# Kernel tuning notes

Hardware: AMD Instinct MI355X
Metric: run time of the kernel (lower is better)

## Reference

```python
import jax, jax.numpy as jnp
import numpy as np

D_MODEL = 1024
NUM_HEADS = 16
WINDOW = 128
DEPTH = D_MODEL // NUM_HEADS


def setup_inputs() -> dict:
    key = jax.random.key(0)
    ks = jax.random.split(key, 9)
    B, S = 2, 2048
    scale = 1.0 / np.sqrt(D_MODEL)
    x = jax.random.normal(ks[0], (B, S, D_MODEL), dtype=jnp.float32)
    Wq = jax.random.normal(ks[1], (D_MODEL, D_MODEL), dtype=jnp.float32) * scale
    Wk = jax.random.normal(ks[2], (D_MODEL, D_MODEL), dtype=jnp.float32) * scale
    Wv = jax.random.normal(ks[3], (D_MODEL, D_MODEL), dtype=jnp.float32) * scale
    Wo = jax.random.normal(ks[4], (D_MODEL, D_MODEL), dtype=jnp.float32) * scale
    bq = jnp.zeros((D_MODEL,), jnp.float32)
    bk = jnp.zeros((D_MODEL,), jnp.float32)
    bv = jnp.zeros((D_MODEL,), jnp.float32)
    bo = jnp.zeros((D_MODEL,), jnp.float32)
    return {"x": x, "Wq": Wq, "bq": bq, "Wk": Wk, "bk": bk,
            "Wv": Wv, "bv": bv, "Wo": Wo, "bo": bo}


def _split_heads(t, B, S):
    # [B,S,D] -> [B,H,S,depth]
    return t.reshape(B, S, NUM_HEADS, DEPTH).transpose(0, 2, 1, 3)


def reference(x, Wq, bq, Wk, bk, Wv, bv, Wo, bo):
    B, S, _ = x.shape
    q = _split_heads(x @ Wq + bq, B, S)
    k = _split_heads(x @ Wk + bk, B, S)
    v = _split_heads(x @ Wv + bv, B, S)
    scores = jnp.einsum('bhqd,bhkd->bhqk', q, k) / jnp.sqrt(jnp.float32(DEPTH))
    idx = jnp.arange(S)
    # mask[i_row=j, i_col=i] per original: |i - j| <= window (symmetric)
    local = jnp.abs(idx[None, :] - idx[:, None]) <= WINDOW  # [S,S]
    scores = jnp.where(local[None, None], scores, jnp.float32(-1e9))
    attn = jax.nn.softmax(scores, axis=-1)
    out = jnp.einsum('bhqk,bhkd->bhqd', attn, v)
    concat = out.transpose(0, 2, 1, 3).reshape(B, S, D_MODEL)
    return concat @ Wo + bo
```

## Files before the change

### kernel.cpp

```cpp
#include <hip/hip_runtime.h>
#include <cstdint>
#include <cstddef>

typedef __attribute__((ext_vector_type(8))) short short8;
typedef __attribute__((ext_vector_type(4))) short short4v;
typedef __attribute__((ext_vector_type(4))) float f32x4;
typedef short8 bf16x8;

typedef __attribute__((address_space(1))) const unsigned GU;
typedef __attribute__((address_space(3))) unsigned LU;

__device__ __forceinline__ short f2bf(float f) {
  unsigned u = __builtin_bit_cast(unsigned, f);
  u += 0x7fffu + ((u >> 16) & 1u);
  return (short)(u >> 16);
}

__global__ __launch_bounds__(256) void k_cast_x(const float* __restrict__ x, short* __restrict__ xb) {
  size_t i = ((size_t)blockIdx.x * 256 + threadIdx.x) * 8;
  f32x4 a = *(const f32x4*)(x + i);
  f32x4 b = *(const f32x4*)(x + i + 4);
  short8 o;
#pragma unroll
  for (int j = 0; j < 4; ++j) { o[j] = f2bf(a[j]); o[4 + j] = f2bf(b[j]); }
  *(short8*)(xb + i) = o;
}

__global__ __launch_bounds__(256) void k_tw(const float* __restrict__ W0, const float* __restrict__ W1,
                                            const float* __restrict__ W2, const float* __restrict__ W3,
                                            short* __restrict__ WT) {
  __shared__ short T[64 * 72];
  int bid = blockIdx.x;
  int widx = bid >> 8;
  int t = bid & 255;
  int kr = (t >> 4) * 64, nc = (t & 15) * 64;
  const float* W = widx == 0 ? W0 : widx == 1 ? W1 : widx == 2 ? W2 : W3;
  short* out = WT + (size_t)widx * 1048576;
  int tid = threadIdx.x;
#pragma unroll
  for (int i = 0; i < 4; ++i) {
    int idx = tid + i * 256;
    int k = idx >> 4, n4 = (idx & 15) << 2;
    f32x4 v = *(const f32x4*)(W + (size_t)(kr + k) * 1024 + nc + n4);
#pragma unroll
    for (int j = 0; j < 4; ++j) T[(n4 + j) * 72 + k] = f2bf(v[j]);
  }
  __syncthreads();
#pragma unroll
  for (int i = 0; i < 2; ++i) {
    int idx = tid + i * 256;
    int n = idx >> 3, k8 = (idx & 7) << 3;
    *(short8*)(out + (size_t)(nc + n) * 1024 + kr + k8) = *(const short8*)&T[n * 72 + k8];
  }
}

__global__ __launch_bounds__(256) void k_tv(const short* __restrict__ v, short* __restrict__ vT) {
  __shared__ short T[64 * 72];
  int bid = blockIdx.x;
  int stile = bid & 31, h = (bid >> 5) & 15, b = bid >> 9;
  int s0 = stile * 64;
  int tid = threadIdx.x;
#pragma unroll
  for (int i = 0; i < 2; ++i) {
    int idx = tid + i * 256;
    int s = idx >> 3, d0 = (idx & 7) << 3;
    short8 vec = *(const short8*)(v + ((size_t)b * 2048 + s0 + s) * 1024 + h * 64 + d0);
#pragma unroll
    for (int j = 0; j < 8; ++j) T[(d0 + j) * 72 + s] = vec[j];
  }
  __syncthreads();
#pragma unroll
  for (int i = 0; i < 2; ++i) {
    int idx = tid + i * 256;
    int d = idx >> 3, s8 = (idx & 7) << 3;
    *(short8*)(vT + (((size_t)b * 16 + h) * 64 + d) * 2048 + s0 + s8) = *(const short8*)&T[d * 72 + s8];
  }
}

template <int MODE>
__global__ __launch_bounds__(256, 2) void k_gemm(
    const short* __restrict__ A, const short* __restrict__ BT,
    const float* __restrict__ bias0, const float* __restrict__ bias1, const float* __restrict__ bias2,
    short* __restrict__ outb, float* __restrict__ outf) {
  __shared__ short As[2][128 * 32];
  __shared__ short Bs[2][128 * 32];
  const int tid = threadIdx.x;
  const int lane = tid & 63, w = tid >> 6;
  const int g = lane >> 4, qi = lane & 15;
  const int wr = (w >> 1) * 64, wc = (w & 1) * 64;
  const int m0 = blockIdx.y * 128, n0 = blockIdx.x * 128;
  const size_t K = 1024;
  const short* Ab = A + (size_t)m0 * K;
  const short* Bb = BT + (size_t)n0 * K;

  auto stage = [&](int buf, int k0) {
#pragma unroll
    for (int i = 0; i < 2; ++i) {
      int cidx = tid + i * 256;
      int r = cidx >> 2, c = (cidx & 3) << 3;
      __builtin_amdgcn_global_load_lds((GU*)(Ab + (size_t)r * K + k0 + c),
                                       (LU*)(&As[buf][cidx * 8]), 16, 0, 0);
      __builtin_amdgcn_global_load_lds((GU*)(Bb + (size_t)r * K + k0 + c),
                                       (LU*)(&Bs[buf][cidx * 8]), 16, 0, 0);
    }
  };

  f32x4 acc[4][4];
#pragma unroll
  for (int i = 0; i < 4; ++i)
#pragma unroll
    for (int j = 0; j < 4; ++j) acc[i][j] = (f32x4)(0.0f);

  stage(0, 0);
  __syncthreads();
  for (int kt = 0; kt < 32; ++kt) {
    int cur = kt & 1;
    if (kt < 31) stage(cur ^ 1, (kt + 1) * 32);
    bf16x8 a[4], b[4];
#pragma unroll
    for (int mf = 0; mf < 4; ++mf)
      a[mf] = *(const bf16x8*)&As[cur][(wr + mf * 16 + qi) * 32 + g * 8];
#pragma unroll
    for (int nf = 0; nf < 4; ++nf)
      b[nf] = *(const bf16x8*)&Bs[cur][(wc + nf * 16 + qi) * 32 + g * 8];
#pragma unroll
    for (int mf = 0; mf < 4; ++mf)
#pragma unroll
      for (int nf = 0; nf < 4; ++nf)
        acc[mf][nf] = __builtin_amdgcn_mfma_f32_16x16x32_bf16(a[mf], b[nf], acc[mf][nf], 0, 0, 0);
    __syncthreads();
  }

  if (MODE == 0) {
    int sel = n0 >> 10;
    const float* bias = sel == 0 ? bias0 : (sel == 1 ? bias1 : bias2);
    size_t outoff = (size_t)sel * 4194304;
#pragma unroll
    for (int nf = 0; nf < 4; ++nf) {
      int col = n0 + wc + nf * 16 + qi;
      int cl = col & 1023;
      float bv = bias[cl];
#pragma unroll
      for (int mf = 0; mf < 4; ++mf) {
        int row = m0 + wr + mf * 16 + g * 4;
#pragma unroll
        for (int j = 0; j < 4; ++j)
          outb[outoff + (size_t)(row + j) * 1024 + cl] = f2bf(acc[mf][nf][j] + bv);
      }
    }
  } else {
#pragma unroll
    for (int nf = 0; nf < 4; ++nf) {
      int col = n0 + wc + nf * 16 + qi;
      float bv = bias0[col];
#pragma unroll
      for (int mf = 0; mf < 4; ++mf) {
        int row = m0 + wr + mf * 16 + g * 4;
#pragma unroll
        for (int j = 0; j < 4; ++j)
          outf[(size_t)(row + j) * 1024 + col] = acc[mf][nf][j] + bv;
      }
    }
  }
}

__global__ __launch_bounds__(256, 2) void k_attn(const short* __restrict__ qg_,
                                                 const short* __restrict__ kg_,
                                                 const short* __restrict__ vT,
                                                 short* __restrict__ outp) {
  __shared__ short Qs[64 * 72];
  __shared__ short Ks[64 * 72];
  __shared__ short Vs[64 * 72];
  __shared__ short Ps[4][16 * 72];
  int bid = blockIdx.x;
  int qt = bid & 31, h = (bid >> 5) & 15, b = bid >> 9;
  int q0 = qt * 64;
  int tid = threadIdx.x, lane = tid & 63, w = tid >> 6;
  int g = lane >> 4, qi = lane & 15;

  const short* qsrc = qg_ + ((size_t)b * 2048 + q0) * 1024 + h * 64;
#pragma unroll
  for (int i = 0; i < 2; ++i) {
    int idx = tid + i * 256;
    int r = idx >> 3, c = (idx & 7) << 3;
    *(short8*)&Qs[r * 72 + c] = *(const short8*)&qsrc[(size_t)r * 1024 + c];
  }

  float m = -1e30f, l = 0.f;
  f32x4 oacc[4];
#pragma unroll
  for (int i = 0; i < 4; ++i) oacc[i] = (f32x4)(0.0f);
  int qglob = q0 + w * 16 + qi;

  for (int cc = 0; cc < 5; ++cc) {
    int kb0 = q0 - 128 + cc * 64;
    if (kb0 < 0 || kb0 >= 2048) continue;
    __syncthreads();
    const short* ksrc = kg_ + ((size_t)b * 2048 + kb0) * 1024 + h * 64;
    const short* vsrc = vT + ((size_t)(b * 16 + h)) * 64 * 2048 + kb0;
#pragma unroll
    for (int i = 0; i < 2; ++i) {
      int idx = tid + i * 256;
      int r = idx >> 3, c = (idx & 7) << 3;
      *(short8*)&Ks[r * 72 + c] = *(const short8*)&ksrc[(size_t)r * 1024 + c];
      *(short8*)&Vs[r * 72 + c] = *(const short8*)&vsrc[(size_t)r * 2048 + c];
    }
    __syncthreads();

    f32x4 st[4];
#pragma unroll
    for (int i = 0; i < 4; ++i) st[i] = (f32x4)(0.0f);
#pragma unroll
    for (int ds = 0; ds < 2; ++ds) {
      bf16x8 qf = *(const bf16x8*)&Qs[(w * 16 + qi) * 72 + ds * 32 + g * 8];
#pragma unroll
      for (int mf = 0; mf < 4; ++mf) {
        bf16x8 kf = *(const bf16x8*)&Ks[(mf * 16 + qi) * 72 + ds * 32 + g * 8];
        st[mf] = __builtin_amdgcn_mfma_f32_16x16x32_bf16(kf, qf, st[mf], 0, 0, 0);
      }
    }

    float pv[16];
    float pm = -1e30f;
#pragma unroll
    for (int mf = 0; mf < 4; ++mf)
#pragma unroll
      for (int j = 0; j < 4; ++j) {
        int kcol = kb0 + mf * 16 + g * 4 + j;
        float s = st[mf][j] * 0.125f;
        int d = kcol - qglob;
        bool valid = (d >= -128) && (d <= 128);
        s = valid ? s : -1e30f;
        pv[mf * 4 + j] = s;
        pm = fmaxf(pm, s);
      }
    pm = fmaxf(pm, __shfl_xor(pm, 16));
    pm = fmaxf(pm, __shfl_xor(pm, 32));
    float mnew = fmaxf(m, pm);
    float scale = __expf(m - mnew);
    float ls = 0.f;
#pragma unroll
    for (int e = 0; e < 16; ++e) {
      float p = pv[e] > -1e29f ? __expf(pv[e] - mnew) : 0.f;
      pv[e] = p;
      ls += p;
    }
    ls += __shfl_xor(ls, 16);
    ls += __shfl_xor(ls, 32);
    l = l * scale + ls;
    m = mnew;
#pragma unroll
    for (int mf = 0; mf < 4; ++mf) oacc[mf] *= scale;

#pragma unroll
    for (int f = 0; f < 4; ++f) {
      short4v pk;
#pragma unroll
      for (int j = 0; j < 4; ++j) pk[j] = f2bf(pv[f * 4 + j]);
      *(short4v*)&Ps[w][qi * 72 + f * 16 + g * 4] = pk;
    }

#pragma unroll
    for (int ks = 0; ks < 2; ++ks) {
      bf16x8 pf = *(const bf16x8*)&Ps[w][qi * 72 + ks * 32 + g * 8];
#pragma unroll
      for (int mf = 0; mf < 4; ++mf) {
        bf16x8 vf = *(const bf16x8*)&Vs[(mf * 16 + qi) * 72 + ks * 32 + g * 8];
        oacc[mf] = __builtin_amdgcn_mfma_f32_16x16x32_bf16(vf, pf, oacc[mf], 0, 0, 0);
      }
    }
  }

  __syncthreads();
  short* Os = Ks;
  float inv = 1.f / l;
#pragma unroll
  for (int mf = 0; mf < 4; ++mf) {
    short4v pk;
#pragma unroll
    for (int j = 0; j < 4; ++j) pk[j] = f2bf(oacc[mf][j] * inv);
    *(short4v*)&Os[(w * 16 + qi) * 72 + mf * 16 + g * 4] = pk;
  }
  __syncthreads();
  short* dst = outp + ((size_t)b * 2048 + q0) * 1024 + h * 64;
  int r = tid >> 2, c16 = (tid & 3) << 4;
  *(short8*)&dst[(size_t)r * 1024 + c16] = *(const short8*)&Os[r * 72 + c16];
  *(short8*)&dst[(size_t)r * 1024 + c16 + 8] = *(const short8*)&Os[r * 72 + c16 + 8];
}

extern "C" void kernel_launch(void* const* d_in, const int* in_sizes, int n_in,
                              void* d_out, int out_size, void* d_ws, size_t ws_size,
                              hipStream_t stream) {
  const float* x  = (const float*)d_in[0];
  const float* Wq = (const float*)d_in[1];
  const float* bq = (const float*)d_in[2];
  const float* Wk = (const float*)d_in[3];
  const float* bk = (const float*)d_in[4];
  const float* Wv = (const float*)d_in[5];
  const float* bv = (const float*)d_in[6];
  const float* Wo = (const float*)d_in[7];
  const float* bo = (const float*)d_in[8];

  short* ws = (short*)d_ws;
  short* xb       = ws;
  short* qkv      = ws + 4194304;
  short* vbuf     = qkv + 2 * 4194304;
  short* vT       = ws;
  short* attn_out = vbuf;
  short* WT       = ws + 4 * 4194304;

  k_cast_x<<<2048, 256, 0, stream>>>(x, xb);
  k_tw<<<1024, 256, 0, stream>>>(Wq, Wk, Wv, Wo, WT);
  {
    dim3 grid(24, 32);
    k_gemm<0><<<grid, 256, 0, stream>>>(xb, WT, bq, bk, bv, qkv, nullptr);
  }
  k_tv<<<1024, 256, 0, stream>>>(vbuf, vT);
  k_attn<<<1024, 256, 0, stream>>>(qkv, qkv + 4194304, vT, attn_out);
  {
    dim3 grid(8, 32);
    k_gemm<1><<<grid, 256, 0, stream>>>(attn_out, WT + 3 * 1048576, bo, bo, bo, nullptr, (float*)d_out);
  }
}
```

Before: 100.4 us.

## Swizzle GEMM LDS tiles and stage epilogue through LDS for coalesced stores

```diff
diff --git a/kernel.cpp b/kernel.cpp
--- a/kernel.cpp
+++ b/kernel.cpp
@@ -82,8 +82,7 @@
     const short* __restrict__ A, const short* __restrict__ BT,
     const float* __restrict__ bias0, const float* __restrict__ bias1, const float* __restrict__ bias2,
     short* __restrict__ outb, float* __restrict__ outf) {
-  __shared__ short As[2][128 * 32];
-  __shared__ short Bs[2][128 * 32];
+  __shared__ short Smem[16384];
   const int tid = threadIdx.x;
   const int lane = tid & 63, w = tid >> 6;
   const int g = lane >> 4, qi = lane & 15;
@@ -94,14 +93,17 @@
   const short* Bb = BT + (size_t)n0 * K;
 
   auto stage = [&](int buf, int k0) {
+    short* Asb = Smem + buf * 4096;
+    short* Bsb = Smem + 8192 + buf * 4096;
 #pragma unroll
     for (int i = 0; i < 2; ++i) {
       int cidx = tid + i * 256;
-      int r = cidx >> 2, c = (cidx & 3) << 3;
-      __builtin_amdgcn_global_load_lds((GU*)(Ab + (size_t)r * K + k0 + c),
-                                       (LU*)(&As[buf][cidx * 8]), 16, 0, 0);
-      __builtin_amdgcn_global_load_lds((GU*)(Bb + (size_t)r * K + k0 + c),
-                                       (LU*)(&Bs[buf][cidx * 8]), 16, 0, 0);
+      int r = cidx >> 2;
+      int csw = ((cidx & 3) ^ ((r >> 1) & 3)) << 3;
+      __builtin_amdgcn_global_load_lds((GU*)(Ab + (size_t)r * K + k0 + csw),
+                                       (LU*)(&Asb[cidx * 8]), 16, 0, 0);
+      __builtin_amdgcn_global_load_lds((GU*)(Bb + (size_t)r * K + k0 + csw),
+                                       (LU*)(&Bsb[cidx * 8]), 16, 0, 0);
     }
   };
 
@@ -116,13 +118,19 @@
   for (int kt = 0; kt < 32; ++kt) {
     int cur = kt & 1;
     if (kt < 31) stage(cur ^ 1, (kt + 1) * 32);
+    const short* Asb = Smem + cur * 4096;
+    const short* Bsb = Smem + 8192 + cur * 4096;
     bf16x8 a[4], b[4];
 #pragma unroll
-    for (int mf = 0; mf < 4; ++mf)
-      a[mf] = *(const bf16x8*)&As[cur][(wr + mf * 16 + qi) * 32 + g * 8];
-#pragma unroll
-    for (int nf = 0; nf < 4; ++nf)
-      b[nf] = *(const bf16x8*)&Bs[cur][(wc + nf * 16 + qi) * 32 + g * 8];
+    for (int mf = 0; mf < 4; ++mf) {
+      int R = wr + mf * 16 + qi;
+      a[mf] = *(const bf16x8*)&Asb[R * 32 + ((g ^ ((R >> 1) & 3)) << 3)];
+    }
+#pragma unroll
+    for (int nf = 0; nf < 4; ++nf) {
+      int R = wc + nf * 16 + qi;
+      b[nf] = *(const bf16x8*)&Bsb[R * 32 + ((g ^ ((R >> 1) & 3)) << 3)];
+    }
 #pragma unroll
     for (int mf = 0; mf < 4; ++mf)
 #pragma unroll
@@ -135,30 +143,48 @@
     int sel = n0 >> 10;
     const float* bias = sel == 0 ? bias0 : (sel == 1 ? bias1 : bias2);
     size_t outoff = (size_t)sel * 4194304;
-#pragma unroll
-    for (int nf = 0; nf < 4; ++nf) {
-      int col = n0 + wc + nf * 16 + qi;
-      int cl = col & 1023;
-      float bv = bias[cl];
-#pragma unroll
-      for (int mf = 0; mf < 4; ++mf) {
-        int row = m0 + wr + mf * 16 + g * 4;
+    int ncol0 = n0 & 1023;
+    float bv[4];
+#pragma unroll
+    for (int nf = 0; nf < 4; ++nf) bv[nf] = bias[ncol0 + wc + nf * 16 + qi];
+    short* Os = Smem;
+#pragma unroll
+    for (int mf = 0; mf < 4; ++mf) {
+      __syncthreads();
+#pragma unroll
+      for (int nf = 0; nf < 4; ++nf)
 #pragma unroll
         for (int j = 0; j < 4; ++j)
-          outb[outoff + (size_t)(row + j) * 1024 + cl] = f2bf(acc[mf][nf][j] + bv);
+          Os[((w >> 1) * 16 + g * 4 + j) * 136 + wc + nf * 16 + qi] = f2bf(acc[mf][nf][j] + bv[nf]);
+      __syncthreads();
+#pragma unroll
+      for (int i = 0; i < 2; ++i) {
+        int idx = tid + i * 256;
+        int r = idx >> 4, c8 = (idx & 15) << 3;
+        int row = m0 + ((r >> 4) << 6) + mf * 16 + (r & 15);
+        *(short8*)&outb[outoff + (size_t)row * 1024 + ncol0 + c8] = *(const short8*)&Os[r * 136 + c8];
       }
     }
   } else {
-#pragma unroll
-    for (int nf = 0; nf < 4; ++nf) {
-      int col = n0 + wc + nf * 16 + qi;
-      float bv = bias0[col];
-#pragma unroll
-      for (int mf = 0; mf < 4; ++mf) {
-        int row = m0 + wr + mf * 16 + g * 4;
+    float* Ft = (float*)Smem;
+    float bv[4];
+#pragma unroll
+    for (int nf = 0; nf < 4; ++nf) bv[nf] = bias0[n0 + wc + nf * 16 + qi];
+#pragma unroll
+    for (int mf = 0; mf < 4; ++mf) {
+      __syncthreads();
+#pragma unroll
+      for (int nf = 0; nf < 4; ++nf)
 #pragma unroll
         for (int j = 0; j < 4; ++j)
-          outf[(size_t)(row + j) * 1024 + col] = acc[mf][nf][j] + bv;
+          Ft[((w >> 1) * 16 + g * 4 + j) * 136 + wc + nf * 16 + qi] = acc[mf][nf][j] + bv[nf];
+      __syncthreads();
+#pragma unroll
+      for (int i = 0; i < 4; ++i) {
+        int idx = tid + i * 256;
+        int r = idx >> 5, c4 = (idx & 31) << 2;
+        int row = m0 + ((r >> 4) << 6) + mf * 16 + (r & 15);
+        *(f32x4*)&outf[(size_t)row * 1024 + n0 + c4] = *(const f32x4*)&Ft[r * 136 + c4];
       }
     }
   }
```

Measured after the change: 96.34 us. -4.1%, faster.
